# Optimization experiments

Measured on AMD Instinct MI355X. Metric: run time of the kernel, lower is better.

Reference implementation:

```python
import jax, jax.numpy as jnp
import numpy as np

GROUPS = 8
HEADS = 4
EPS = 1e-5


def setup_inputs() -> dict:
    key = jax.random.key(0)
    ks = jax.random.split(key, 3)
    b, c, h, w = 4, 256, 64, 64
    x = jax.random.normal(ks[0], (b, c, h, w), dtype=jnp.float32)
    gn_gamma = jnp.ones((c,), jnp.float32)
    gn_beta = jnp.zeros((c,), jnp.float32)
    w_qkv = jax.random.normal(ks[1], (3 * c, c), dtype=jnp.float32) * (c ** -0.5)
    w_proj = jax.random.normal(ks[2], (c, c), dtype=jnp.float32) * (c ** -0.5)
    b_proj = jnp.zeros((c,), jnp.float32)
    return {"x": x, "gn_gamma": gn_gamma, "gn_beta": gn_beta,
            "w_qkv": w_qkv, "w_proj": w_proj, "b_proj": b_proj}


def reference(x, gn_gamma, gn_beta, w_qkv, w_proj, b_proj):
    b, c, h, w = x.shape
    residual = x
    # GroupNorm(8, c)
    xg = x.reshape(b, GROUPS, -1)
    mean = jnp.mean(xg, axis=-1, keepdims=True)
    var = jnp.var(xg, axis=-1, keepdims=True)
    xn = ((xg - mean) * jax.lax.rsqrt(var + EPS)).reshape(b, c, h, w)
    xn = xn * gn_gamma[:, None, None] + gn_beta[:, None, None]
    # QKV conv1x1 (no bias)
    qkv = jnp.einsum('oc,bchw->bohw', w_qkv, xn)  # [b,3c,h,w]
    q, k, v = jnp.split(qkv, 3, axis=1)
    n = h * w
    dh = c // HEADS
    q = q.reshape(b, HEADS, dh, n)
    k = k.reshape(b, HEADS, dh, n)
    v = v.reshape(b, HEADS, dh, n)
    scale = (c * HEADS) ** (-0.5)
    attn = jnp.einsum('bhci,bhcj->bhij', q, k) * scale  # [b,H,n,n]
    attn = jax.nn.softmax(attn, axis=-1)
    out = jnp.einsum('bhij,bhcj->bhci', attn, v).reshape(b, c, h, w)
    out = jnp.einsum('oc,bchw->bohw', w_proj, out) + b_proj[:, None, None]
    return out + residual
```

## Files before the change

### kernel.cpp

```cpp
#include <hip/hip_runtime.h>
#include <math.h>
#include <stdint.h>

#define B_ 4
#define C_ 256
#define HW_ 4096
#define G_ 8
#define H_ 4
#define DH_ 64
#define GRP_ELEMS (32 * HW_)
#define NCHUNK 16
#define CHUNK_ELEMS (GRP_ELEMS / NCHUNK)
#define EPS 1e-5f
#define NT_ (HW_ / 64)
#define QSCALE 0.04508422f

typedef __attribute__((ext_vector_type(8))) short short8;
typedef __attribute__((ext_vector_type(4))) float f32x4;
typedef __attribute__((ext_vector_type(4))) unsigned int u32x4;
typedef const __attribute__((address_space(1))) uint32_t* gas1_t;
typedef __attribute__((address_space(3))) uint32_t* las3_t;

__device__ __forceinline__ ushort f2bf(float x) {
    unsigned u = __builtin_bit_cast(unsigned, x);
    u += 0x7FFFu + ((u >> 16) & 1u);
    return (ushort)(u >> 16);
}
__device__ __forceinline__ uint32_t cvt_pk_bf16(float lo, float hi) {
    uint32_t r;
    asm("v_cvt_pk_bf16_f32 %0, %1, %2" : "=v"(r) : "v"(lo), "v"(hi));
    return r;
}

__global__ __launch_bounds__(256) void gn_partial(const float* __restrict__ x,
                                                  float* __restrict__ part) {
    int bg = blockIdx.x >> 4;
    int chunk = blockIdx.x & 15;
    const float4* p = (const float4*)(x + (size_t)bg * GRP_ELEMS + (size_t)chunk * CHUNK_ELEMS);
    int t = threadIdx.x;
    float s = 0.f, ss = 0.f;
#pragma unroll
    for (int i = 0; i < 8; ++i) {
        float4 v = p[t + i * 256];
        s  += v.x + v.y + v.z + v.w;
        ss += v.x * v.x + v.y * v.y + v.z * v.z + v.w * v.w;
    }
#pragma unroll
    for (int off = 32; off; off >>= 1) {
        s  += __shfl_xor(s, off, 64);
        ss += __shfl_xor(ss, off, 64);
    }
    __shared__ float ls[8];
    int wave = t >> 6, lane = t & 63;
    if (lane == 0) { ls[wave * 2] = s; ls[wave * 2 + 1] = ss; }
    __syncthreads();
    if (t == 0) {
        float S = 0.f, SS = 0.f;
#pragma unroll
        for (int w = 0; w < 4; ++w) { S += ls[w * 2]; SS += ls[w * 2 + 1]; }
        part[(bg * 16 + chunk) * 2]     = S;
        part[(bg * 16 + chunk) * 2 + 1] = SS;
    }
}

__global__ __launch_bounds__(256) void wcvt(const float* __restrict__ wq,
                                            const float* __restrict__ wp,
                                            ushort* __restrict__ wqb,
                                            ushort* __restrict__ wpb) {
    int i = blockIdx.x * 256 + threadIdx.x;
    if (i < 768 * 256) {
        float s = (i < 256 * 256) ? QSCALE : 1.0f;
        wqb[i] = f2bf(wq[i] * s);
    } else {
        int j = i - 768 * 256;
        wpb[j] = f2bf(wp[j]);
    }
}

__global__ __launch_bounds__(256) void gn_xt(const float* __restrict__ x,
                                             const float* __restrict__ gamma,
                                             const float* __restrict__ beta,
                                             const float* __restrict__ part,
                                             ushort* __restrict__ xnT) {
    __shared__ float2 affs[64];
    __shared__ __align__(16) ushort Ts[64 * 72];
    int n0 = blockIdx.x * 64;
    int c0 = blockIdx.y * 64;
    int b  = blockIdx.z;
    int t = threadIdx.x;
    if (t < 64) {
        int c = c0 + t;
        int bg = b * G_ + (c >> 5);
        float S = 0.f, SS = 0.f;
#pragma unroll
        for (int i = 0; i < 16; ++i) {
            S  += part[(bg * 16 + i) * 2];
            SS += part[(bg * 16 + i) * 2 + 1];
        }
        float mean = S * (1.f / GRP_ELEMS);
        float var  = SS * (1.f / GRP_ELEMS) - mean * mean;
        float inv  = rsqrtf(var + EPS);
        float a = inv * gamma[c];
        affs[t] = make_float2(a, beta[c] - mean * a);
    }
    __syncthreads();
    int n4 = t & 15, cr = t >> 4;
#pragma unroll
    for (int ct = 0; ct < 4; ++ct) {
        int c = cr + 16 * ct;
        float2 p = affs[c];
        float4 v = *(const float4*)(x + ((size_t)(b * C_ + c0 + c)) * HW_ + n0 + n4 * 4);
        ushort e[4];
        e[0] = f2bf(v.x * p.x + p.y); e[1] = f2bf(v.y * p.x + p.y);
        e[2] = f2bf(v.z * p.x + p.y); e[3] = f2bf(v.w * p.x + p.y);
#pragma unroll
        for (int k = 0; k < 4; ++k) {
            int n = n4 * 4 + k;
            Ts[n * 72 + (((c >> 3) ^ ((n >> 2) & 7)) << 3) + (c & 7)] = e[k];
        }
    }
    __syncthreads();
#pragma unroll
    for (int nt = 0; nt < 2; ++nt) {
        int n = (t >> 3) + 32 * nt, c8 = t & 7;
        uint4 val = *(const uint4*)&Ts[n * 72 + ((c8 ^ ((n >> 2) & 7)) << 3)];
        *(uint4*)(xnT + ((size_t)b * HW_ + n0 + n) * C_ + c0 + c8 * 8) = val;
    }
}

__global__ __launch_bounds__(256) void qkv_gemm(const ushort* __restrict__ wqb,
                                                const ushort* __restrict__ xnT,
                                                ushort* __restrict__ qt,
                                                ushort* __restrict__ kt,
                                                ushort* __restrict__ vv) {
    int n0 = blockIdx.x * 64;
    int o0 = blockIdx.y * 128;
    int b  = blockIdx.z;
    int t = threadIdx.x;
    int w = t >> 6, lane = t & 63, l16 = lane & 15, lg = lane >> 4;
    const ushort* xb = xnT + ((size_t)b * HW_ + n0) * C_;
    const ushort* wrow0 = wqb + (size_t)(o0 + 32 * w + l16) * C_;
    const ushort* wrow1 = wrow0 + 16 * C_;

    f32x4 acc[2][4];
#pragma unroll
    for (int os = 0; os < 2; ++os)
#pragma unroll
        for (int u = 0; u < 4; ++u)
#pragma unroll
            for (int r = 0; r < 4; ++r) acc[os][u][r] = 0.f;

#pragma unroll 2
    for (int ks = 0; ks < 8; ++ks) {
        short8 a0 = *(const short8*)(wrow0 + 32 * ks + 8 * lg);
        short8 a1 = *(const short8*)(wrow1 + 32 * ks + 8 * lg);
#pragma unroll
        for (int u = 0; u < 4; ++u) {
            short8 bf = *(const short8*)(xb + (size_t)(16 * u + l16) * C_ + 32 * ks + 8 * lg);
            acc[0][u] = __builtin_amdgcn_mfma_f32_16x16x32_bf16(a0, bf, acc[0][u], 0, 0, 0);
            acc[1][u] = __builtin_amdgcn_mfma_f32_16x16x32_bf16(a1, bf, acc[1][u], 0, 0, 0);
        }
    }

    int z = o0 >> 8;
#pragma unroll
    for (int os = 0; os < 2; ++os) {
        int o_base = o0 + 32 * w + 16 * os;
        if (z < 2) {
            int h = (o_base >> 6) & 3;
            int od0 = (o_base & 63) + 4 * lg;
            ushort* dstb = (z ? kt : qt) + ((size_t)((b << 2) | h) * HW_) * DH_;
#pragma unroll
            for (int u = 0; u < 4; ++u) {
                int n = n0 + 16 * u + l16;
                uint2 pk;
                pk.x = cvt_pk_bf16(acc[os][u][0], acc[os][u][1]);
                pk.y = cvt_pk_bf16(acc[os][u][2], acc[os][u][3]);
                *(uint2*)(dstb + (size_t)n * DH_ + od0) = pk;
            }
        } else {
            int row0 = o_base - 512 + 4 * lg;
#pragma unroll
            for (int u = 0; u < 4; ++u) {
                int n = n0 + 16 * u + l16;
#pragma unroll
                for (int r = 0; r < 4; ++r)
                    vv[((size_t)(b * C_ + row0 + r)) * HW_ + n] = f2bf(acc[os][u][r]);
            }
        }
    }
}

__global__ __launch_bounds__(256) void flash_attn_mfma(const ushort* __restrict__ qt,
                                                       const ushort* __restrict__ kt,
                                                       const ushort* __restrict__ vv,
                                                       ushort* __restrict__ attT) {
    __shared__ __align__(16) ushort Kb[4][64 * 64];
    __shared__ __align__(16) ushort Vb[4][64 * 64];

    int bid = blockIdx.x;
    int wg = (bid & 7) * 64 + (bid >> 3);
    int bh = wg >> 5;
    int i0 = (wg & 31) * 128;
    int b = bh >> 2, h = bh & 3;
    int t = threadIdx.x;
    int w = t >> 6, lane = t & 63, l16 = lane & 15, lg = lane >> 4;
    const ushort* qtb = qt + (size_t)bh * HW_ * DH_;
    const ushort* ktb = kt + (size_t)bh * HW_ * DH_;
    const ushort* vb  = vv + ((size_t)(b * C_) + h * DH_) * HW_;

    short8 qf[2][2];
#pragma unroll
    for (int s = 0; s < 2; ++s)
#pragma unroll
        for (int ks = 0; ks < 2; ++ks)
            qf[s][ks] = *(const short8*)(qtb + (size_t)(i0 + 32 * w + 16 * s + l16) * DH_ + 32 * ks + 8 * lg);

    f32x4 O0[4], O1[4], lacc0, lacc1;
#pragma unroll
    for (int dt = 0; dt < 4; ++dt)
#pragma unroll
        for (int r = 0; r < 4; ++r) { O0[dt][r] = 0.f; O1[dt][r] = 0.f; }
#pragma unroll
    for (int r = 0; r < 4; ++r) { lacc0[r] = 0.f; lacc1[r] = 0.f; }

    u32x4 ov; ov[0] = ov[1] = ov[2] = ov[3] = 0x3F803F80u;
    short8 onesf = __builtin_bit_cast(short8, ov);

    int r8 = lane >> 3, ch8 = lane & 7;
    size_t koff[2], voff[2];
#pragma unroll
    for (int half = 0; half < 2; ++half) {
        int L = 16 * w + half * 8 + r8;
        int gk = (L & 0x23) | ((L & 0x0C) << 1) | ((L & 0x10) >> 2);
        koff[half] = (size_t)gk * DH_ + ((ch8 ^ (L & 7)) << 3);
        voff[half] = (size_t)L * HW_ + ((ch8 ^ (L & 7)) << 3);
    }

    auto stageK = [&](int bi, int j0) {
#pragma unroll
        for (int half = 0; half < 2; ++half) {
            int rowb = 16 * w + half * 8;
            __builtin_amdgcn_global_load_lds((gas1_t)(ktb + (size_t)j0 * DH_ + koff[half]),
                (las3_t)&Kb[bi][rowb * 64], 16, 0, 0);
        }
    };
    auto stageV = [&](int bi, int j0) {
#pragma unroll
        for (int half = 0; half < 2; ++half) {
            int rowb = 16 * w + half * 8;
            __builtin_amdgcn_global_load_lds((gas1_t)(vb + (size_t)j0 + voff[half]),
                (las3_t)&Vb[bi][rowb * 64], 16, 0, 0);
        }
    };

    auto qk2 = [&](int bi, f32x4* S0, f32x4* S1) {
        __builtin_amdgcn_s_setprio(1);
#pragma unroll
        for (int jt = 0; jt < 4; ++jt) {
#pragma unroll
            for (int r = 0; r < 4; ++r) { S0[jt][r] = 0.f; S1[jt][r] = 0.f; }
#pragma unroll
            for (int ks = 0; ks < 2; ++ks) {
                short8 kf = *(const short8*)&Kb[bi][(16 * jt + l16) * 64 +
                                                    (((4 * ks + lg) ^ (l16 & 7)) << 3)];
                S0[jt] = __builtin_amdgcn_mfma_f32_16x16x32_bf16(kf, qf[0][ks], S0[jt], 0, 0, 0);
                S1[jt] = __builtin_amdgcn_mfma_f32_16x16x32_bf16(kf, qf[1][ks], S1[jt], 0, 0, 0);
            }
        }
        __builtin_amdgcn_s_setprio(0);
    };

    auto pv2 = [&](int bi, short8* pf0, short8* pf1) {
        __builtin_amdgcn_s_setprio(1);
#pragma unroll
        for (int dt = 0; dt < 4; ++dt) {
#pragma unroll
            for (int ks = 0; ks < 2; ++ks) {
                short8 vf = *(const short8*)&Vb[bi][(16 * dt + l16) * 64 +
                                                    (((4 * ks + lg) ^ (l16 & 7)) << 3)];
                O0[dt] = __builtin_amdgcn_mfma_f32_16x16x32_bf16(vf, pf0[ks], O0[dt], 0, 0, 0);
                O1[dt] = __builtin_amdgcn_mfma_f32_16x16x32_bf16(vf, pf1[ks], O1[dt], 0, 0, 0);
            }
        }
        lacc0 = __builtin_amdgcn_mfma_f32_16x16x32_bf16(onesf, pf0[0], lacc0, 0, 0, 0);
        lacc0 = __builtin_amdgcn_mfma_f32_16x16x32_bf16(onesf, pf0[1], lacc0, 0, 0, 0);
        lacc1 = __builtin_amdgcn_mfma_f32_16x16x32_bf16(onesf, pf1[0], lacc1, 0, 0, 0);
        lacc1 = __builtin_amdgcn_mfma_f32_16x16x32_bf16(onesf, pf1[1], lacc1, 0, 0, 0);
        __builtin_amdgcn_s_setprio(0);
    };

    auto softmax_pf = [&](f32x4* S, short8* pf) {
#pragma unroll
        for (int jt = 0; jt < 4; ++jt)
#pragma unroll
            for (int r = 0; r < 4; ++r)
                S[jt][r] = __builtin_amdgcn_exp2f(S[jt][r]);
#pragma unroll
        for (int ks = 0; ks < 2; ++ks) {
            u32x4 p;
            p[0] = cvt_pk_bf16(S[2 * ks][0],     S[2 * ks][1]);
            p[1] = cvt_pk_bf16(S[2 * ks][2],     S[2 * ks][3]);
            p[2] = cvt_pk_bf16(S[2 * ks + 1][0], S[2 * ks + 1][1]);
            p[3] = cvt_pk_bf16(S[2 * ks + 1][2], S[2 * ks + 1][3]);
            pf[ks] = __builtin_bit_cast(short8, p);
        }
    };

    f32x4 Sa0[4], Sa1[4], Sb0[4], Sb1[4];

    auto body = [&](int VW, int KR, int KW, int VR,
                    f32x4* SC0, f32x4* SC1, f32x4* SN0, f32x4* SN1,
                    int tt, int drain) {
        if (tt + 2 < NT_) stageV(VW, (tt + 2) * 64);
        qk2(KR, SN0, SN1);
        if (tt + 3 < NT_) stageK(KW, (tt + 3) * 64);
        short8 pf0[2], pf1[2];
        softmax_pf(SC0, pf0);
        softmax_pf(SC1, pf1);
        pv2(VR, pf0, pf1);
        if (drain == 8)      asm volatile("s_waitcnt vmcnt(8)" ::: "memory");
        else if (drain == 4) asm volatile("s_waitcnt vmcnt(4)" ::: "memory");
        else                 asm volatile("s_waitcnt vmcnt(0)" ::: "memory");
        __builtin_amdgcn_s_barrier();
    };

    stageK(0, 0); stageV(0, 0);
    stageK(1, 64); stageV(1, 128 - 64);
    stageK(2, 128);
    asm volatile("s_waitcnt vmcnt(0)" ::: "memory");
    __builtin_amdgcn_s_barrier();
    qk2(0, Sa0, Sa1);

    for (int g = 0; g < 15; ++g) {
        int tb = 4 * g;
        body(2, 1, 3, 0, Sa0, Sa1, Sb0, Sb1, tb + 0, 8);
        body(3, 2, 0, 1, Sb0, Sb1, Sa0, Sa1, tb + 1, 8);
        body(0, 3, 1, 2, Sa0, Sa1, Sb0, Sb1, tb + 2, 8);
        body(1, 0, 2, 3, Sb0, Sb1, Sa0, Sa1, tb + 3, 8);
    }
    body(2, 1, 3, 0, Sa0, Sa1, Sb0, Sb1, 60, 8);
    body(3, 2, 0, 1, Sb0, Sb1, Sa0, Sa1, 61, 4);
    body(0, 3, 1, 2, Sa0, Sa1, Sb0, Sb1, 62, 0);
    {
        short8 pf0[2], pf1[2];
        softmax_pf(Sb0, pf0);
        softmax_pf(Sb1, pf1);
        pv2(3, pf0, pf1);
    }

    float inv0 = 1.f / lacc0[0], inv1 = 1.f / lacc1[0];
    ushort* ab0 = attT + ((size_t)b * HW_ + i0 + 32 * w + l16) * C_ + h * DH_;
    ushort* ab1 = ab0 + 16 * C_;
#pragma unroll
    for (int dt = 0; dt < 4; ++dt) {
        uint2 p0, p1;
        p0.x = cvt_pk_bf16(O0[dt][0] * inv0, O0[dt][1] * inv0);
        p0.y = cvt_pk_bf16(O0[dt][2] * inv0, O0[dt][3] * inv0);
        *(uint2*)(ab0 + 16 * dt + 4 * lg) = p0;
        p1.x = cvt_pk_bf16(O1[dt][0] * inv1, O1[dt][1] * inv1);
        p1.y = cvt_pk_bf16(O1[dt][2] * inv1, O1[dt][3] * inv1);
        *(uint2*)(ab1 + 16 * dt + 4 * lg) = p1;
    }
}

__global__ __launch_bounds__(256) void proj_gemm(const ushort* __restrict__ wpb,
                                                 const ushort* __restrict__ attT,
                                                 const float* __restrict__ bias,
                                                 const float* __restrict__ x,
                                                 float* __restrict__ out) {
    int n0 = blockIdx.x * 64;
    int o0 = blockIdx.y * 128;
    int b  = blockIdx.z;
    int t = threadIdx.x;
    int w = t >> 6, lane = t & 63, l16 = lane & 15, lg = lane >> 4;
    const ushort* xb = attT + ((size_t)b * HW_ + n0) * C_;
    const ushort* wrow0 = wpb + (size_t)(o0 + 32 * w + l16) * C_;
    const ushort* wrow1 = wrow0 + 16 * C_;

    f32x4 acc[2][4];
#pragma unroll
    for (int os = 0; os < 2; ++os)
#pragma unroll
        for (int u = 0; u < 4; ++u)
#pragma unroll
            for (int r = 0; r < 4; ++r) acc[os][u][r] = 0.f;

#pragma unroll 2
    for (int ks = 0; ks < 8; ++ks) {
        short8 a0 = *(const short8*)(wrow0 + 32 * ks + 8 * lg);
        short8 a1 = *(const short8*)(wrow1 + 32 * ks + 8 * lg);
#pragma unroll
        for (int u = 0; u < 4; ++u) {
            short8 bf = *(const short8*)(xb + (size_t)(16 * u + l16) * C_ + 32 * ks + 8 * lg);
            acc[0][u] = __builtin_amdgcn_mfma_f32_16x16x32_bf16(a0, bf, acc[0][u], 0, 0, 0);
            acc[1][u] = __builtin_amdgcn_mfma_f32_16x16x32_bf16(a1, bf, acc[1][u], 0, 0, 0);
        }
    }

#pragma unroll
    for (int os = 0; os < 2; ++os) {
        int o_base = o0 + 32 * w + 16 * os;
#pragma unroll
        for (int u = 0; u < 4; ++u) {
            int n = n0 + 16 * u + l16;
#pragma unroll
            for (int r = 0; r < 4; ++r) {
                int mrow = o_base + 4 * lg + r;
                size_t idx = ((size_t)(b * C_ + mrow)) * HW_ + n;
                out[idx] = acc[os][u][r] + bias[mrow] + x[idx];
            }
        }
    }
}

extern "C" void kernel_launch(void* const* d_in, const int* in_sizes, int n_in,
                              void* d_out, int out_size, void* d_ws, size_t ws_size,
                              hipStream_t stream) {
    const float* x        = (const float*)d_in[0];
    const float* gn_gamma = (const float*)d_in[1];
    const float* gn_beta  = (const float*)d_in[2];
    const float* w_qkv    = (const float*)d_in[3];
    const float* w_proj   = (const float*)d_in[4];
    const float* b_proj   = (const float*)d_in[5];
    float* out = (float*)d_out;

    ushort* wsp  = (ushort*)d_ws;
    ushort* xnT  = wsp;
    ushort* qt   = xnT  + 4194304;
    ushort* kt   = qt   + 4194304;
    ushort* vv   = kt   + 4194304;
    ushort* attT = vv   + 4194304;
    ushort* wqb  = attT + 4194304;
    ushort* wpb  = wqb  + 196608;
    float*  part = (float*)(wpb + 65536);

    gn_partial<<<dim3(G_ * B_ * NCHUNK), 256, 0, stream>>>(x, part);
    wcvt<<<dim3(1024), 256, 0, stream>>>(w_qkv, w_proj, wqb, wpb);
    gn_xt<<<dim3(HW_ / 64, C_ / 64, B_), 256, 0, stream>>>(x, gn_gamma, gn_beta, part, xnT);
    qkv_gemm<<<dim3(HW_ / 64, 6, B_), 256, 0, stream>>>(wqb, xnT, qt, kt, vv);
    flash_attn_mfma<<<dim3(512), 256, 0, stream>>>(qt, kt, vv, attT);
    proj_gemm<<<dim3(HW_ / 64, 2, B_), 256, 0, stream>>>(wpb, attT, b_proj, x, out);
}
```

Measured before the change: 142.8 us.

## Fuse GroupNorm apply and transpose into QKV GEMM via shared memory

Merges the gn_xt and qkv_gemm kernels. Each block normalizes a 64-pixel by 256-channel tile into LDS, then computes all 768 QKV outputs from that LDS tile. This drops the xnT global round trip and one launch. In exchange there are only 256 blocks, more LDS per block and serial z iterations, so occupancy may be lower. It also tidies flash attention QK: the first MFMA now accumulates into a zero constant instead of explicitly zeroing S, and the stageV offset is rewritten without changing its value.

```diff
diff --git a/kernel.cpp b/kernel.cpp
--- a/kernel.cpp
+++ b/kernel.cpp
@@ -77,19 +77,23 @@
     }
 }
 
-__global__ __launch_bounds__(256) void gn_xt(const float* __restrict__ x,
-                                             const float* __restrict__ gamma,
-                                             const float* __restrict__ beta,
-                                             const float* __restrict__ part,
-                                             ushort* __restrict__ xnT) {
-    __shared__ float2 affs[64];
-    __shared__ __align__(16) ushort Ts[64 * 72];
+#define TSTR 264
+__global__ __launch_bounds__(256) void gn_qkv(const float* __restrict__ x,
+                                              const float* __restrict__ gamma,
+                                              const float* __restrict__ beta,
+                                              const float* __restrict__ part,
+                                              const ushort* __restrict__ wqb,
+                                              ushort* __restrict__ qt,
+                                              ushort* __restrict__ kt,
+                                              ushort* __restrict__ vv) {
+    __shared__ float2 affs[256];
+    __shared__ __align__(16) ushort Ts[64 * TSTR];
     int n0 = blockIdx.x * 64;
-    int c0 = blockIdx.y * 64;
-    int b  = blockIdx.z;
+    int b  = blockIdx.y;
     int t = threadIdx.x;
-    if (t < 64) {
-        int c = c0 + t;
+
+    {
+        int c = t;
         int bg = b * G_ + (c >> 5);
         float S = 0.f, SS = 0.f;
 #pragma unroll
@@ -101,93 +105,89 @@
         float var  = SS * (1.f / GRP_ELEMS) - mean * mean;
         float inv  = rsqrtf(var + EPS);
         float a = inv * gamma[c];
-        affs[t] = make_float2(a, beta[c] - mean * a);
+        affs[c] = make_float2(a, beta[c] - mean * a);
     }
     __syncthreads();
-    int n4 = t & 15, cr = t >> 4;
-#pragma unroll
-    for (int ct = 0; ct < 4; ++ct) {
-        int c = cr + 16 * ct;
-        float2 p = affs[c];
-        float4 v = *(const float4*)(x + ((size_t)(b * C_ + c0 + c)) * HW_ + n0 + n4 * 4);
-        ushort e[4];
-        e[0] = f2bf(v.x * p.x + p.y); e[1] = f2bf(v.y * p.x + p.y);
-        e[2] = f2bf(v.z * p.x + p.y); e[3] = f2bf(v.w * p.x + p.y);
-#pragma unroll
-        for (int k = 0; k < 4; ++k) {
-            int n = n4 * 4 + k;
-            Ts[n * 72 + (((c >> 3) ^ ((n >> 2) & 7)) << 3) + (c & 7)] = e[k];
+
+    {
+        int n4 = t & 15, cr = t >> 4;
+#pragma unroll
+        for (int ct = 0; ct < 16; ++ct) {
+            int c = cr + 16 * ct;
+            float2 p = affs[c];
+            float4 v = *(const float4*)(x + ((size_t)(b * C_ + c)) * HW_ + n0 + n4 * 4);
+            ushort e[4];
+            e[0] = f2bf(v.x * p.x + p.y); e[1] = f2bf(v.y * p.x + p.y);
+            e[2] = f2bf(v.z * p.x + p.y); e[3] = f2bf(v.w * p.x + p.y);
+#pragma unroll
+            for (int k = 0; k < 4; ++k) {
+                int n = n4 * 4 + k;
+                Ts[n * TSTR + (((c >> 3) ^ ((n >> 2) & 7)) << 3) + (c & 7)] = e[k];
+            }
         }
     }
     __syncthreads();
-#pragma unroll
-    for (int nt = 0; nt < 2; ++nt) {
-        int n = (t >> 3) + 32 * nt, c8 = t & 7;
-        uint4 val = *(const uint4*)&Ts[n * 72 + ((c8 ^ ((n >> 2) & 7)) << 3)];
-        *(uint4*)(xnT + ((size_t)b * HW_ + n0 + n) * C_ + c0 + c8 * 8) = val;
-    }
-}
-
-__global__ __launch_bounds__(256) void qkv_gemm(const ushort* __restrict__ wqb,
-                                                const ushort* __restrict__ xnT,
-                                                ushort* __restrict__ qt,
-                                                ushort* __restrict__ kt,
-                                                ushort* __restrict__ vv) {
-    int n0 = blockIdx.x * 64;
-    int o0 = blockIdx.y * 128;
-    int b  = blockIdx.z;
-    int t = threadIdx.x;
+
     int w = t >> 6, lane = t & 63, l16 = lane & 15, lg = lane >> 4;
-    const ushort* xb = xnT + ((size_t)b * HW_ + n0) * C_;
-    const ushort* wrow0 = wqb + (size_t)(o0 + 32 * w + l16) * C_;
-    const ushort* wrow1 = wrow0 + 16 * C_;
-
-    f32x4 acc[2][4];
-#pragma unroll
-    for (int os = 0; os < 2; ++os)
-#pragma unroll
-        for (int u = 0; u < 4; ++u)
-#pragma unroll
-            for (int r = 0; r < 4; ++r) acc[os][u][r] = 0.f;
+
+    for (int z = 0; z < 3; ++z) {
+        const ushort* wz = wqb + (size_t)(z * 256 + 32 * w + l16) * C_;
+        f32x4 acc[2][2][4];
+#pragma unroll
+        for (int j = 0; j < 2; ++j)
+#pragma unroll
+            for (int os = 0; os < 2; ++os)
+#pragma unroll
+                for (int u = 0; u < 4; ++u)
+#pragma unroll
+                    for (int r = 0; r < 4; ++r) acc[j][os][u][r] = 0.f;
 
 #pragma unroll 2
-    for (int ks = 0; ks < 8; ++ks) {
-        short8 a0 = *(const short8*)(wrow0 + 32 * ks + 8 * lg);
-        short8 a1 = *(const short8*)(wrow1 + 32 * ks + 8 * lg);
-#pragma unroll
-        for (int u = 0; u < 4; ++u) {
-            short8 bf = *(const short8*)(xb + (size_t)(16 * u + l16) * C_ + 32 * ks + 8 * lg);
-            acc[0][u] = __builtin_amdgcn_mfma_f32_16x16x32_bf16(a0, bf, acc[0][u], 0, 0, 0);
-            acc[1][u] = __builtin_amdgcn_mfma_f32_16x16x32_bf16(a1, bf, acc[1][u], 0, 0, 0);
-        }
-    }
-
-    int z = o0 >> 8;
-#pragma unroll
-    for (int os = 0; os < 2; ++os) {
-        int o_base = o0 + 32 * w + 16 * os;
-        if (z < 2) {
-            int h = (o_base >> 6) & 3;
-            int od0 = (o_base & 63) + 4 * lg;
-            ushort* dstb = (z ? kt : qt) + ((size_t)((b << 2) | h) * HW_) * DH_;
+        for (int ks = 0; ks < 8; ++ks) {
+            short8 a00 = *(const short8*)(wz + 32 * ks + 8 * lg);
+            short8 a01 = *(const short8*)(wz + 16 * C_ + 32 * ks + 8 * lg);
+            short8 a10 = *(const short8*)(wz + 128 * C_ + 32 * ks + 8 * lg);
+            short8 a11 = *(const short8*)(wz + 144 * C_ + 32 * ks + 8 * lg);
 #pragma unroll
             for (int u = 0; u < 4; ++u) {
-                int n = n0 + 16 * u + l16;
-                uint2 pk;
-                pk.x = cvt_pk_bf16(acc[os][u][0], acc[os][u][1]);
-                pk.y = cvt_pk_bf16(acc[os][u][2], acc[os][u][3]);
-                *(uint2*)(dstb + (size_t)n * DH_ + od0) = pk;
+                int n = 16 * u + l16;
+                short8 bf = *(const short8*)&Ts[n * TSTR +
+                               (((4 * ks + lg) ^ ((n >> 2) & 7)) << 3)];
+                acc[0][0][u] = __builtin_amdgcn_mfma_f32_16x16x32_bf16(a00, bf, acc[0][0][u], 0, 0, 0);
+                acc[0][1][u] = __builtin_amdgcn_mfma_f32_16x16x32_bf16(a01, bf, acc[0][1][u], 0, 0, 0);
+                acc[1][0][u] = __builtin_amdgcn_mfma_f32_16x16x32_bf16(a10, bf, acc[1][0][u], 0, 0, 0);
+                acc[1][1][u] = __builtin_amdgcn_mfma_f32_16x16x32_bf16(a11, bf, acc[1][1][u], 0, 0, 0);
             }
-        } else {
-            int row0 = o_base - 512 + 4 * lg;
-#pragma unroll
-            for (int u = 0; u < 4; ++u) {
-                int n = n0 + 16 * u + l16;
-#pragma unroll
-                for (int r = 0; r < 4; ++r)
-                    vv[((size_t)(b * C_ + row0 + r)) * HW_ + n] = f2bf(acc[os][u][r]);
+        }
+
+#pragma unroll
+        for (int j = 0; j < 2; ++j)
+#pragma unroll
+            for (int os = 0; os < 2; ++os) {
+                int o_base = z * 256 + 128 * j + 32 * w + 16 * os;
+                if (z < 2) {
+                    int h = (o_base >> 6) & 3;
+                    int od0 = (o_base & 63) + 4 * lg;
+                    ushort* dstb = (z ? kt : qt) + ((size_t)((b << 2) | h) * HW_) * DH_;
+#pragma unroll
+                    for (int u = 0; u < 4; ++u) {
+                        int n = n0 + 16 * u + l16;
+                        uint2 pk;
+                        pk.x = cvt_pk_bf16(acc[j][os][u][0], acc[j][os][u][1]);
+                        pk.y = cvt_pk_bf16(acc[j][os][u][2], acc[j][os][u][3]);
+                        *(uint2*)(dstb + (size_t)n * DH_ + od0) = pk;
+                    }
+                } else {
+                    int row0 = o_base - 512 + 4 * lg;
+#pragma unroll
+                    for (int u = 0; u < 4; ++u) {
+                        int n = n0 + 16 * u + l16;
+#pragma unroll
+                        for (int r = 0; r < 4; ++r)
+                            vv[((size_t)(b * C_ + row0 + r)) * HW_ + n] = f2bf(acc[j][os][u][r]);
+                    }
+                }
             }
-        }
     }
 }
 
@@ -223,6 +223,7 @@
         for (int r = 0; r < 4; ++r) { O0[dt][r] = 0.f; O1[dt][r] = 0.f; }
 #pragma unroll
     for (int r = 0; r < 4; ++r) { lacc0[r] = 0.f; lacc1[r] = 0.f; }
+    const f32x4 Z4 = {0.f, 0.f, 0.f, 0.f};
 
     u32x4 ov; ov[0] = ov[1] = ov[2] = ov[3] = 0x3F803F80u;
     short8 onesf = __builtin_bit_cast(short8, ov);
@@ -258,15 +259,14 @@
         __builtin_amdgcn_s_setprio(1);
 #pragma unroll
         for (int jt = 0; jt < 4; ++jt) {
-#pragma unroll
-            for (int r = 0; r < 4; ++r) { S0[jt][r] = 0.f; S1[jt][r] = 0.f; }
-#pragma unroll
-            for (int ks = 0; ks < 2; ++ks) {
-                short8 kf = *(const short8*)&Kb[bi][(16 * jt + l16) * 64 +
-                                                    (((4 * ks + lg) ^ (l16 & 7)) << 3)];
-                S0[jt] = __builtin_amdgcn_mfma_f32_16x16x32_bf16(kf, qf[0][ks], S0[jt], 0, 0, 0);
-                S1[jt] = __builtin_amdgcn_mfma_f32_16x16x32_bf16(kf, qf[1][ks], S1[jt], 0, 0, 0);
-            }
+            short8 kf0 = *(const short8*)&Kb[bi][(16 * jt + l16) * 64 +
+                                                ((lg ^ (l16 & 7)) << 3)];
+            S0[jt] = __builtin_amdgcn_mfma_f32_16x16x32_bf16(kf0, qf[0][0], Z4, 0, 0, 0);
+            S1[jt] = __builtin_amdgcn_mfma_f32_16x16x32_bf16(kf0, qf[1][0], Z4, 0, 0, 0);
+            short8 kf1 = *(const short8*)&Kb[bi][(16 * jt + l16) * 64 +
+                                                (((4 + lg) ^ (l16 & 7)) << 3)];
+            S0[jt] = __builtin_amdgcn_mfma_f32_16x16x32_bf16(kf1, qf[0][1], S0[jt], 0, 0, 0);
+            S1[jt] = __builtin_amdgcn_mfma_f32_16x16x32_bf16(kf1, qf[1][1], S1[jt], 0, 0, 0);
         }
         __builtin_amdgcn_s_setprio(0);
     };
@@ -326,18 +326,17 @@
     };
 
     stageK(0, 0); stageV(0, 0);
-    stageK(1, 64); stageV(1, 128 - 64);
+    stageK(1, 64); stageV(1, 64);
     stageK(2, 128);
     asm volatile("s_waitcnt vmcnt(0)" ::: "memory");
     __builtin_amdgcn_s_barrier();
     qk2(0, Sa0, Sa1);
 
     for (int g = 0; g < 15; ++g) {
-        int tb = 4 * g;
-        body(2, 1, 3, 0, Sa0, Sa1, Sb0, Sb1, tb + 0, 8);
-        body(3, 2, 0, 1, Sb0, Sb1, Sa0, Sa1, tb + 1, 8);
-        body(0, 3, 1, 2, Sa0, Sa1, Sb0, Sb1, tb + 2, 8);
-        body(1, 0, 2, 3, Sb0, Sb1, Sa0, Sa1, tb + 3, 8);
+        body(2, 1, 3, 0, Sa0, Sa1, Sb0, Sb1, 4 * g + 0, 8);
+        body(3, 2, 0, 1, Sb0, Sb1, Sa0, Sa1, 4 * g + 1, 8);
+        body(0, 3, 1, 2, Sa0, Sa1, Sb0, Sb1, 4 * g + 2, 8);
+        body(1, 0, 2, 3, Sb0, Sb1, Sa0, Sa1, 4 * g + 3, 8);
     }
     body(2, 1, 3, 0, Sa0, Sa1, Sb0, Sb1, 60, 8);
     body(3, 2, 0, 1, Sb0, Sb1, Sa0, Sa1, 61, 4);
@@ -426,8 +425,7 @@
     float* out = (float*)d_out;
 
     ushort* wsp  = (ushort*)d_ws;
-    ushort* xnT  = wsp;
-    ushort* qt   = xnT  + 4194304;
+    ushort* qt   = wsp;
     ushort* kt   = qt   + 4194304;
     ushort* vv   = kt   + 4194304;
     ushort* attT = vv   + 4194304;
@@ -437,8 +435,7 @@
 
     gn_partial<<<dim3(G_ * B_ * NCHUNK), 256, 0, stream>>>(x, part);
     wcvt<<<dim3(1024), 256, 0, stream>>>(w_qkv, w_proj, wqb, wpb);
-    gn_xt<<<dim3(HW_ / 64, C_ / 64, B_), 256, 0, stream>>>(x, gn_gamma, gn_beta, part, xnT);
-    qkv_gemm<<<dim3(HW_ / 64, 6, B_), 256, 0, stream>>>(wqb, xnT, qt, kt, vv);
+    gn_qkv<<<dim3(HW_ / 64, B_), 256, 0, stream>>>(x, gn_gamma, gn_beta, part, wqb, qt, kt, vv);
     flash_attn_mfma<<<dim3(512), 256, 0, stream>>>(qt, kt, vv, attT);
     proj_gemm<<<dim3(HW_ / 64, 2, B_), 256, 0, stream>>>(wpb, attT, b_proj, x, out);
 }
```

Measured after the change: 122.2 us. 1.17x faster.
